# Performance work log

Measured on AMD Instinct MI355X. Metric: run time of the kernel, lower is better.

## Reference

```python
import jax, jax.numpy as jnp
import numpy as np

COUNT, L1, L2, L3 = 8, 3072, 15, 32


def setup_inputs() -> dict:
    key = jax.random.key(0)
    ks = jax.random.split(key, 10)
    B = 16384
    x = jax.random.uniform(ks[0], (B, L1), dtype=jnp.float32)
    ls_indices = jax.random.randint(ks[1], (B,), 0, COUNT, dtype=jnp.int32)
    s = 1.0 / np.sqrt(L1)
    l1_w = jax.random.uniform(ks[2], (COUNT * (L2 + 1), L1), minval=-s, maxval=s, dtype=jnp.float32)
    l1_b = jax.random.uniform(ks[3], (COUNT * (L2 + 1),), minval=-s, maxval=s, dtype=jnp.float32)
    # l1_fact initialized to zero in the module; use small random values for a
    # meaningful numeric test (same math either way)
    l1f_w = 0.01 * jax.random.normal(ks[4], (L2 + 1, L1), dtype=jnp.float32)
    l1f_b = 0.01 * jax.random.normal(ks[5], (L2 + 1,), dtype=jnp.float32)
    s2 = 1.0 / np.sqrt(2 * L2)
    l2_w = jax.random.uniform(ks[6], (COUNT * L3, 2 * L2), minval=-s2, maxval=s2, dtype=jnp.float32)
    l2_b = jax.random.uniform(ks[7], (COUNT * L3,), minval=-s2, maxval=s2, dtype=jnp.float32)
    s3 = 1.0 / np.sqrt(L3)
    out_w = jax.random.uniform(ks[8], (COUNT, L3), minval=-s3, maxval=s3, dtype=jnp.float32)
    out_b = jnp.zeros((COUNT,), dtype=jnp.float32)
    return {"x": x, "ls_indices": ls_indices, "l1_w": l1_w, "l1_b": l1_b,
            "l1f_w": l1f_w, "l1f_b": l1f_b, "l2_w": l2_w, "l2_b": l2_b,
            "out_w": out_w, "out_b": out_b}


def _gather_bucket(dense, idx):
    # dense: [B, count, F]; idx: [B] -> [B, F]
    return jnp.take_along_axis(dense, idx[:, None, None], axis=1)[:, 0, :]


def reference(x, ls_indices, l1_w, l1_b, l1f_w, l1f_b, l2_w, l2_b, out_w, out_b):
    B = x.shape[0]
    idx = ls_indices.reshape(-1)
    # L1 stage: dense over all buckets, then gather selected bucket
    l1s = (x @ l1_w.T + l1_b).reshape(B, COUNT, L2 + 1)
    l1c = _gather_bucket(l1s, idx)                      # [B, L2+1]
    l1f = x @ l1f_w.T + l1f_b                           # [B, L2+1]
    l1c_main, l1c_out = l1c[:, :L2], l1c[:, L2:]
    l1f_main, l1f_out = l1f[:, :L2], l1f[:, L2:]
    l1x = l1c_main + l1f_main
    # squared-clipped-ReLU pair: [x^2 * 127/128, x] clamped to [0,1]
    l1x = jnp.clip(jnp.concatenate([jnp.square(l1x) * (127.0 / 128.0), l1x], axis=1), 0.0, 1.0)
    # L2 stage
    l2s = (l1x @ l2_w.T + l2_b).reshape(B, COUNT, L3)
    l2x = jnp.clip(_gather_bucket(l2s, idx), 0.0, 1.0)  # [B, L3]
    # output stage
    l3s = (l2x @ out_w.T + out_b).reshape(B, COUNT, 1)
    l3c = _gather_bucket(l3s, idx)                      # [B, 1]
    return l3c + l1f_out + l1c_out
```

## Files before the change

kernel.cpp:

```cpp
#include <hip/hip_runtime.h>
#include <stdint.h>

#define CNT 8
#define L1D 3072
#define NB 16384
#define BM 64
#define BN 128
#define BK 64
#define KITERS (L1D / BK)
#define LSTR 72

typedef float  float4v  __attribute__((ext_vector_type(4)));
typedef short  short8   __attribute__((ext_vector_type(8)));
typedef unsigned short ushort4v __attribute__((ext_vector_type(4)));

__device__ __forceinline__ unsigned short f2bf(float f) {
  uint32_t u = __builtin_bit_cast(uint32_t, f);
  u += 0x7fffu + ((u >> 16) & 1u);
  return (unsigned short)(u >> 16);
}

__global__ void prep_kernel(const float* __restrict__ l1w, const float* __restrict__ l1b,
                            const float* __restrict__ l1fw, const float* __restrict__ l1fb,
                            unsigned short* __restrict__ cw, float* __restrict__ cb) {
  const int n = blockIdx.y;
  const int k = blockIdx.x * 256 + threadIdx.x;
  cw[n * L1D + k] = f2bf(l1w[n * L1D + k] + l1fw[(n & 15) * L1D + k]);
  if (blockIdx.x == 0 && n == 0 && threadIdx.x < 128)
    cb[threadIdx.x] = l1b[threadIdx.x] + l1fb[threadIdx.x & 15];
}

union __align__(16) SMem {
  struct {
    unsigned short A[2][BM * LSTR];
    unsigned short B[2][BN * LSTR];
  } st;
  struct {
    float yg[BM][20];
    float l2w[960 * 9];
    float outw[256];
    float l2b[256];
    float bias[128];
    int   buck[BM];
  } ep;
};

__global__ __launch_bounds__(256, 1) void fused_kernel(
    const float* __restrict__ x, const int* __restrict__ lsi,
    const unsigned short* __restrict__ cw, const float* __restrict__ cb,
    const float* __restrict__ gl2w, const float* __restrict__ gl2b,
    const float* __restrict__ goutw, const float* __restrict__ goutb,
    float* __restrict__ out) {
  __shared__ SMem sm;
  const int tid  = threadIdx.x;
  const int lane = tid & 63;
  const int wid  = tid >> 6;
  const int mw   = wid & 1;
  const int nw   = wid >> 1;
  const int rowbase = blockIdx.x * BM;

  const int ar = tid >> 4, af = tid & 15;
  const int br = tid >> 3, bc = tid & 7;
  const float* xp = x + (size_t)(rowbase + ar) * L1D + af * 4;
  const unsigned short* wp = cw + (size_t)br * L1D + bc * 8;

  float4v aR[4];
  short8  bR[4];
  float4v acc[2][4];
#pragma unroll
  for (int i = 0; i < 2; ++i)
#pragma unroll
    for (int j = 0; j < 4; ++j) acc[i][j] = float4v{0.f, 0.f, 0.f, 0.f};

#pragma unroll
  for (int p = 0; p < 4; ++p) {
    aR[p] = *(const float4v*)(xp + (size_t)p * 16 * L1D);
    bR[p] = *(const short8*)(wp + (size_t)p * 32 * L1D);
  }
#pragma unroll
  for (int p = 0; p < 4; ++p) {
    ushort4v v = {f2bf(aR[p].x), f2bf(aR[p].y), f2bf(aR[p].z), f2bf(aR[p].w)};
    *(ushort4v*)&sm.st.A[0][(p * 16 + ar) * LSTR + af * 4] = v;
    *(short8*)&sm.st.B[0][(p * 32 + br) * LSTR + bc * 8] = bR[p];
  }
  __syncthreads();

  for (int it = 0; it < KITERS; ++it) {
    const int buf = it & 1;
    if (it + 1 < KITERS) {
      const int koff = (it + 1) * BK;
#pragma unroll
      for (int p = 0; p < 4; ++p) {
        aR[p] = *(const float4v*)(xp + (size_t)p * 16 * L1D + koff);
        bR[p] = *(const short8*)(wp + (size_t)p * 32 * L1D + koff);
      }
    }
#pragma unroll
    for (int ks = 0; ks < 2; ++ks) {
      const int kk = ks * 32 + (lane >> 4) * 8;
      short8 afr[2], bfr[4];
#pragma unroll
      for (int i = 0; i < 2; ++i)
        afr[i] = *(const short8*)&sm.st.A[buf][((2 * mw + i) * 16 + (lane & 15)) * LSTR + kk];
#pragma unroll
      for (int j = 0; j < 4; ++j)
        bfr[j] = *(const short8*)&sm.st.B[buf][((4 * nw + j) * 16 + (lane & 15)) * LSTR + kk];
#pragma unroll
      for (int i = 0; i < 2; ++i)
#pragma unroll
        for (int j = 0; j < 4; ++j)
          acc[i][j] = __builtin_amdgcn_mfma_f32_16x16x32_bf16(afr[i], bfr[j], acc[i][j], 0, 0, 0);
    }
    if (it + 1 < KITERS) {
#pragma unroll
      for (int p = 0; p < 4; ++p) {
        ushort4v v = {f2bf(aR[p].x), f2bf(aR[p].y), f2bf(aR[p].z), f2bf(aR[p].w)};
        *(ushort4v*)&sm.st.A[buf ^ 1][(p * 16 + ar) * LSTR + af * 4] = v;
        *(short8*)&sm.st.B[buf ^ 1][(p * 32 + br) * LSTR + bc * 8] = bR[p];
      }
      __syncthreads();
    }
  }
  __syncthreads();

  if (tid < 64)  sm.ep.buck[tid] = lsi[rowbase + tid];
  if (tid < 128) sm.ep.bias[tid] = cb[tid];
  {
    const int b2 = tid >> 5, n2 = tid & 31;
    sm.ep.outw[n2 * 8 + b2] = goutw[tid];
    sm.ep.l2b[tid] = gl2b[tid];
  }
  for (int i = tid; i < 960 * 8; i += 256) {
    const int b = i / 960;
    const int rem = i - b * 960;
    sm.ep.l2w[rem * 9 + b] = gl2w[i];
  }
  __syncthreads();

#pragma unroll
  for (int i = 0; i < 2; ++i)
#pragma unroll
    for (int j = 0; j < 4; ++j) {
      const int nt = 4 * nw + j;
#pragma unroll
      for (int rg = 0; rg < 4; ++rg) {
        const int r = (2 * mw + i) * 16 + (lane >> 4) * 4 + rg;
        if (sm.ep.buck[r] == nt) sm.ep.yg[r][lane & 15] = acc[i][j][rg];
      }
    }
  __syncthreads();

  {
    const int r = tid >> 2, q = tid & 3;
    const int b = sm.ep.buck[r];
    float act[30];
#pragma unroll
    for (int c = 0; c < 15; ++c) {
      const float v = sm.ep.yg[r][c] + sm.ep.bias[b * 16 + c];
      act[c]      = fminf(v * v * (127.0f / 128.0f), 1.0f);
      act[15 + c] = fminf(fmaxf(v, 0.0f), 1.0f);
    }
    const float y15 = sm.ep.yg[r][15] + sm.ep.bias[b * 16 + 15];
    float o = 0.0f;
#pragma unroll
    for (int nn = 0; nn < 8; ++nn) {
      const int n = q * 8 + nn;
      float s = sm.ep.l2b[b * 32 + n];
#pragma unroll
      for (int k = 0; k < 30; ++k) s += act[k] * sm.ep.l2w[(n * 30 + k) * 9 + b];
      s = fminf(fmaxf(s, 0.0f), 1.0f);
      o += s * sm.ep.outw[n * 8 + b];
    }
    o += __shfl_down(o, 2, 4);
    o += __shfl_down(o, 1, 4);
    if (q == 0) out[rowbase + r] = o + y15 + goutb[b];
  }
}

extern "C" void kernel_launch(void* const* d_in, const int* in_sizes, int n_in,
                              void* d_out, int out_size, void* d_ws, size_t ws_size,
                              hipStream_t stream) {
  const float* x    = (const float*)d_in[0];
  const int*   lsi  = (const int*)d_in[1];
  const float* l1w  = (const float*)d_in[2];
  const float* l1b  = (const float*)d_in[3];
  const float* l1fw = (const float*)d_in[4];
  const float* l1fb = (const float*)d_in[5];
  const float* l2w  = (const float*)d_in[6];
  const float* l2b  = (const float*)d_in[7];
  const float* outw = (const float*)d_in[8];
  const float* outb = (const float*)d_in[9];
  float* out = (float*)d_out;

  unsigned short* cw = (unsigned short*)d_ws;
  float* cb = (float*)((char*)d_ws + 128 * L1D * sizeof(unsigned short));

  prep_kernel<<<dim3(12, 128), 256, 0, stream>>>(l1w, l1b, l1fw, l1fb, cw, cb);
  fused_kernel<<<NB / BM, 256, 0, stream>>>(x, lsi, cw, cb, l2w, l2b, outw, outb, out);
}
```

Measured before the change: 315.5 us.

## Halve row tile to 32 and run two blocks per CU

Shrinks the M tile from 64 to 32 rows so the grid has twice as many blocks, and changes launch bounds to allow two resident blocks per CU. The four waves now split only along N, each computing a 32x32 output patch, and the epilogue uses eight threads per row with a three-step shuffle reduction. The aim is more parallelism and better latency hiding for the memory-bound x stream. The cost is that the weight tile is reloaded from L2 twice as often per row and MFMA work per LDS load drops.

```diff
diff --git a/kernel.cpp b/kernel.cpp
--- a/kernel.cpp
+++ b/kernel.cpp
@@ -4,7 +4,7 @@
 #define CNT 8
 #define L1D 3072
 #define NB 16384
-#define BM 64
+#define BM 32
 #define BN 128
 #define BK 64
 #define KITERS (L1D / BK)
@@ -45,7 +45,7 @@
   } ep;
 };
 
-__global__ __launch_bounds__(256, 1) void fused_kernel(
+__global__ __launch_bounds__(256, 2) void fused_kernel(
     const float* __restrict__ x, const int* __restrict__ lsi,
     const unsigned short* __restrict__ cw, const float* __restrict__ cb,
     const float* __restrict__ gl2w, const float* __restrict__ gl2b,
@@ -55,8 +55,6 @@
   const int tid  = threadIdx.x;
   const int lane = tid & 63;
   const int wid  = tid >> 6;
-  const int mw   = wid & 1;
-  const int nw   = wid >> 1;
   const int rowbase = blockIdx.x * BM;
 
   const int ar = tid >> 4, af = tid & 15;
@@ -64,25 +62,26 @@
   const float* xp = x + (size_t)(rowbase + ar) * L1D + af * 4;
   const unsigned short* wp = cw + (size_t)br * L1D + bc * 8;
 
-  float4v aR[4];
+  float4v aR[2];
   short8  bR[4];
-  float4v acc[2][4];
+  float4v acc[2][2];
 #pragma unroll
   for (int i = 0; i < 2; ++i)
 #pragma unroll
-    for (int j = 0; j < 4; ++j) acc[i][j] = float4v{0.f, 0.f, 0.f, 0.f};
-
-#pragma unroll
-  for (int p = 0; p < 4; ++p) {
-    aR[p] = *(const float4v*)(xp + (size_t)p * 16 * L1D);
-    bR[p] = *(const short8*)(wp + (size_t)p * 32 * L1D);
-  }
-#pragma unroll
-  for (int p = 0; p < 4; ++p) {
+    for (int j = 0; j < 2; ++j) acc[i][j] = float4v{0.f, 0.f, 0.f, 0.f};
+
+#pragma unroll
+  for (int p = 0; p < 2; ++p) aR[p] = *(const float4v*)(xp + (size_t)p * 16 * L1D);
+#pragma unroll
+  for (int p = 0; p < 4; ++p) bR[p] = *(const short8*)(wp + (size_t)p * 32 * L1D);
+#pragma unroll
+  for (int p = 0; p < 2; ++p) {
     ushort4v v = {f2bf(aR[p].x), f2bf(aR[p].y), f2bf(aR[p].z), f2bf(aR[p].w)};
     *(ushort4v*)&sm.st.A[0][(p * 16 + ar) * LSTR + af * 4] = v;
+  }
+#pragma unroll
+  for (int p = 0; p < 4; ++p)
     *(short8*)&sm.st.B[0][(p * 32 + br) * LSTR + bc * 8] = bR[p];
-  }
   __syncthreads();
 
   for (int it = 0; it < KITERS; ++it) {
@@ -90,40 +89,41 @@
     if (it + 1 < KITERS) {
       const int koff = (it + 1) * BK;
 #pragma unroll
-      for (int p = 0; p < 4; ++p) {
-        aR[p] = *(const float4v*)(xp + (size_t)p * 16 * L1D + koff);
-        bR[p] = *(const short8*)(wp + (size_t)p * 32 * L1D + koff);
-      }
+      for (int p = 0; p < 2; ++p) aR[p] = *(const float4v*)(xp + (size_t)p * 16 * L1D + koff);
+#pragma unroll
+      for (int p = 0; p < 4; ++p) bR[p] = *(const short8*)(wp + (size_t)p * 32 * L1D + koff);
     }
 #pragma unroll
     for (int ks = 0; ks < 2; ++ks) {
       const int kk = ks * 32 + (lane >> 4) * 8;
-      short8 afr[2], bfr[4];
+      short8 afr[2], bfr[2];
 #pragma unroll
       for (int i = 0; i < 2; ++i)
-        afr[i] = *(const short8*)&sm.st.A[buf][((2 * mw + i) * 16 + (lane & 15)) * LSTR + kk];
-#pragma unroll
-      for (int j = 0; j < 4; ++j)
-        bfr[j] = *(const short8*)&sm.st.B[buf][((4 * nw + j) * 16 + (lane & 15)) * LSTR + kk];
+        afr[i] = *(const short8*)&sm.st.A[buf][(i * 16 + (lane & 15)) * LSTR + kk];
+#pragma unroll
+      for (int j = 0; j < 2; ++j)
+        bfr[j] = *(const short8*)&sm.st.B[buf][((wid * 2 + j) * 16 + (lane & 15)) * LSTR + kk];
 #pragma unroll
       for (int i = 0; i < 2; ++i)
 #pragma unroll
-        for (int j = 0; j < 4; ++j)
+        for (int j = 0; j < 2; ++j)
           acc[i][j] = __builtin_amdgcn_mfma_f32_16x16x32_bf16(afr[i], bfr[j], acc[i][j], 0, 0, 0);
     }
     if (it + 1 < KITERS) {
 #pragma unroll
-      for (int p = 0; p < 4; ++p) {
+      for (int p = 0; p < 2; ++p) {
         ushort4v v = {f2bf(aR[p].x), f2bf(aR[p].y), f2bf(aR[p].z), f2bf(aR[p].w)};
         *(ushort4v*)&sm.st.A[buf ^ 1][(p * 16 + ar) * LSTR + af * 4] = v;
+      }
+#pragma unroll
+      for (int p = 0; p < 4; ++p)
         *(short8*)&sm.st.B[buf ^ 1][(p * 32 + br) * LSTR + bc * 8] = bR[p];
-      }
       __syncthreads();
     }
   }
   __syncthreads();
 
-  if (tid < 64)  sm.ep.buck[tid] = lsi[rowbase + tid];
+  if (tid < BM)  sm.ep.buck[tid] = lsi[rowbase + tid];
   if (tid < 128) sm.ep.bias[tid] = cb[tid];
   {
     const int b2 = tid >> 5, n2 = tid & 31;
@@ -140,18 +140,18 @@
 #pragma unroll
   for (int i = 0; i < 2; ++i)
 #pragma unroll
-    for (int j = 0; j < 4; ++j) {
-      const int nt = 4 * nw + j;
+    for (int j = 0; j < 2; ++j) {
+      const int nt = wid * 2 + j;
 #pragma unroll
       for (int rg = 0; rg < 4; ++rg) {
-        const int r = (2 * mw + i) * 16 + (lane >> 4) * 4 + rg;
+        const int r = i * 16 + (lane >> 4) * 4 + rg;
         if (sm.ep.buck[r] == nt) sm.ep.yg[r][lane & 15] = acc[i][j][rg];
       }
     }
   __syncthreads();
 
   {
-    const int r = tid >> 2, q = tid & 3;
+    const int r = tid >> 3, q = tid & 7;
     const int b = sm.ep.buck[r];
     float act[30];
 #pragma unroll
@@ -163,16 +163,17 @@
     const float y15 = sm.ep.yg[r][15] + sm.ep.bias[b * 16 + 15];
     float o = 0.0f;
 #pragma unroll
-    for (int nn = 0; nn < 8; ++nn) {
-      const int n = q * 8 + nn;
+    for (int nn = 0; nn < 4; ++nn) {
+      const int n = q * 4 + nn;
       float s = sm.ep.l2b[b * 32 + n];
 #pragma unroll
       for (int k = 0; k < 30; ++k) s += act[k] * sm.ep.l2w[(n * 30 + k) * 9 + b];
       s = fminf(fmaxf(s, 0.0f), 1.0f);
       o += s * sm.ep.outw[n * 8 + b];
     }
-    o += __shfl_down(o, 2, 4);
-    o += __shfl_down(o, 1, 4);
+    o += __shfl_down(o, 4, 8);
+    o += __shfl_down(o, 2, 8);
+    o += __shfl_down(o, 1, 8);
     if (q == 0) out[rowbase + r] = o + y15 + goutb[b];
   }
 }
```

Result: no change. 314.4 us (-0.4%).
